# Performance work log

Hardware: AMD Instinct MI355X
Metric: run time of the kernel (lower is better)

## Reference

```python
import jax, jax.numpy as jnp
import numpy as np

B, L, H, N, CIN, COUT, U = 32, 12, 12, 2048, 2, 1, 64
K3 = 3  # num_matrices = n_supports * max_diffusion_step + 1 = 1*2 + 1


def setup_inputs() -> dict:
    rng = np.random.default_rng(0)
    # random sparse-ish symmetric adjacency -> scaled laplacian support (lambda_max ~= 2)
    A = rng.random((N, N), dtype=np.float32)
    A = np.maximum(A, A.T)
    A = A * (A > 0.995)
    d = A.sum(axis=1)
    dis = 1.0 / np.sqrt(np.maximum(d, 1e-6))
    Lap = np.eye(N, dtype=np.float32) - (dis[:, None] * A) * dis[None, :]
    support = (Lap - np.eye(N, dtype=np.float32)).astype(np.float32)  # 2/lmax*L - I with lmax=2

    key = jax.random.key(0)
    ks = jax.random.split(key, 6)

    def w(k, shape, fan):
        return jax.random.normal(k, shape, jnp.float32) / np.float32(np.sqrt(fan))

    Cg_e = (CIN + U) * K3   # 198
    Cg_d = (COUT + U) * K3  # 195
    return {
        "history_data": jax.random.normal(ks[0], (B, L, N, CIN), jnp.float32),
        "support": jnp.asarray(support),
        "enc_Wg": w(ks[1], (Cg_e, 2 * U), Cg_e),
        "enc_bg": jnp.ones((2 * U,), jnp.float32),  # gate bias starts at 1.0 (original repo)
        "enc_Wc": w(ks[2], (Cg_e, U), Cg_e),
        "enc_bc": jnp.zeros((U,), jnp.float32),
        "dec_Wg": w(ks[3], (Cg_d, 2 * U), Cg_d),
        "dec_bg": jnp.ones((2 * U,), jnp.float32),
        "dec_Wc": w(ks[4], (Cg_d, U), Cg_d),
        "dec_bc": jnp.zeros((U,), jnp.float32),
        "Wp": w(ks[5], (U, COUT), U),
        "bp": jnp.zeros((COUT,), jnp.float32),
    }


def _gconv(support, x, W, b):
    # x: [B, N, C]; Chebyshev diffusion T0=x, T1=Sx, T2=2S(Sx)-x, stacked feature-major
    x1 = jnp.einsum('mn,bnc->bmc', support, x)
    x2 = 2.0 * jnp.einsum('mn,bnc->bmc', support, x1) - x
    xs = jnp.stack([x, x1, x2], axis=-1)  # [B, N, C, 3]
    b_, n_, c_, k_ = xs.shape
    y = xs.reshape(b_ * n_, c_ * k_) @ W + b
    return y.reshape(b_, n_, -1)


def _cell(support, x, h, Wg, bg, Wc, bc):
    # DCGRU cell: x [B,N,in], h [B,N,U]
    cat = jnp.concatenate([x, h], axis=-1)
    ru = jax.nn.sigmoid(_gconv(support, cat, Wg, bg))
    r, u = jnp.split(ru, 2, axis=-1)
    c = jnp.tanh(_gconv(support, jnp.concatenate([x, r * h], axis=-1), Wc, bc))
    return u * h + (1.0 - u) * c


def reference(history_data, support, enc_Wg, enc_bg, enc_Wc, enc_bc,
              dec_Wg, dec_bg, dec_Wc, dec_bc, Wp, bp):
    hist = jnp.transpose(history_data, (1, 0, 2, 3))  # [L, B, N, CIN]
    h0 = jnp.zeros((B, N, U), history_data.dtype)

    def enc_step(h, xt):
        return _cell(support, xt, h, enc_Wg, enc_bg, enc_Wc, enc_bc), None

    h_enc, _ = jax.lax.scan(enc_step, h0, hist)

    go = jnp.zeros((B, N, COUT), history_data.dtype)

    def dec_step(carry, _):
        h, xin = carry
        h = _cell(support, xin, h, dec_Wg, dec_bg, dec_Wc, dec_bc)
        out = (h.reshape(-1, U) @ Wp + bp).reshape(B, N, COUT)
        return (h, out), out

    _, outs = jax.lax.scan(dec_step, (h_enc, go), None, length=H)  # [H, B, N, COUT]
    return jnp.transpose(outs, (1, 0, 2, 3))  # [B, H, N, COUT]
```

## Files before the change

### kernel.cpp

```cpp
#include <hip/hip_runtime.h>
#include <math.h>

#define NN 2048
#define BB 32
#define LL 12
#define HHH 12
#define UU 64
#define STR 68
#define SLAB (BB*STR)
#define SEGS 8
#define SEGW (SLAB/SEGS)
#define MR (NN*BB)
#define CSR_CAP 262144
#define PACK_HALF 28672

typedef short bfrag __attribute__((ext_vector_type(8)));
typedef float ffrag __attribute__((ext_vector_type(4)));

__device__ __forceinline__ float sigm(float x) { return 1.0f / (1.0f + __expf(-x)); }
__device__ __forceinline__ float tanhfast(float x) {
  float e = __expf(2.0f * x);
  return 1.0f - 2.0f / (e + 1.0f);
}

__device__ __forceinline__ void cvt8(const float* a, bfrag* hi, bfrag* lo) {
  bfrag H, L;
  #pragma unroll
  for (int j = 0; j < 8; ++j) {
    unsigned u = __float_as_uint(a[j]);
    unsigned hb = (u + 0x7FFFu + ((u >> 16) & 1u)) >> 16;
    float rem = a[j] - __uint_as_float(hb << 16);
    unsigned u2 = __float_as_uint(rem);
    unsigned lb = (u2 + 0x7FFFu + ((u2 >> 16) & 1u)) >> 16;
    H[j] = (short)hb; L[j] = (short)lb;
  }
  *hi = H; *lo = L;
}

__global__ __launch_bounds__(256) void k_row_count(const float* __restrict__ S, int* __restrict__ cnt) {
  int m = blockIdx.x;
  const float* row = S + (size_t)m * NN;
  int c = 0;
  for (int i = threadIdx.x; i < NN; i += 256) c += (row[i] != 0.0f);
  __shared__ int sm[4];
  for (int off = 32; off; off >>= 1) c += __shfl_down(c, off, 64);
  if ((threadIdx.x & 63) == 0) sm[threadIdx.x >> 6] = c;
  __syncthreads();
  if (threadIdx.x == 0) cnt[m] = sm[0] + sm[1] + sm[2] + sm[3];
}

__global__ __launch_bounds__(256) void k_scan(const int* __restrict__ cnt, int* __restrict__ rp) {
  __shared__ int tot[256];
  int t = threadIdx.x;
  int base = t * 8;
  int v[8]; int s = 0;
  #pragma unroll
  for (int k = 0; k < 8; ++k) { v[k] = cnt[base + k]; s += v[k]; }
  tot[t] = s;
  __syncthreads();
  for (int off = 1; off < 256; off <<= 1) {
    int add = (t >= off) ? tot[t - off] : 0;
    __syncthreads();
    tot[t] += add;
    __syncthreads();
  }
  int run = (t == 0) ? 0 : tot[t - 1];
  #pragma unroll
  for (int k = 0; k < 8; ++k) { rp[base + k] = run; run += v[k]; }
  if (t == 255) rp[NN] = run;
}

__global__ __launch_bounds__(256) void k_fill(const float* __restrict__ S, const int* __restrict__ rp,
                                              int* __restrict__ cols, float* __restrict__ vals) {
  int m = blockIdx.x;
  const float* row = S + (size_t)m * NN;
  __shared__ int wsum[4];
  __shared__ int chunkbase;
  if (threadIdx.x == 0) chunkbase = rp[m];
  __syncthreads();
  int lane = threadIdx.x & 63, w = threadIdx.x >> 6;
  for (int ch = 0; ch < NN / 256; ++ch) {
    int i = ch * 256 + threadIdx.x;
    float val = row[i];
    bool p = (val != 0.0f);
    unsigned long long mask = __ballot(p);
    int rank = __popcll(mask & ((1ull << lane) - 1ull));
    if (lane == 0) wsum[w] = __popcll(mask);
    __syncthreads();
    int off = 0;
    for (int q = 0; q < w; ++q) off += wsum[q];
    if (p) { int k = chunkbase + off + rank; cols[k] = i * SLAB; vals[k] = val; }
    __syncthreads();
    if (threadIdx.x == 0) chunkbase += wsum[0] + wsum[1] + wsum[2] + wsum[3];
    __syncthreads();
  }
}

__global__ __launch_bounds__(256) void k_pack(const float* __restrict__ Wsrc, unsigned short* __restrict__ dst,
                                              int CIN_, int NO) {
  int idx = blockIdx.x * 256 + threadIdx.x;
  int nh_count = NO >> 6;
  int tot = nh_count * 7 * 4 * 64 * 8;
  if (idx >= tot) return;
  int j = idx & 7;
  int r1 = idx >> 3;  int lane = r1 & 63;
  int r2 = r1 >> 6;   int nf = r2 & 3;
  int r3 = r2 >> 2;   int ks = r3 % 7; int nh = r3 / 7;
  int grp = lane >> 4, l15 = lane & 15;
  int col = nh*64 + nf*16 + l15;
  float wv = 0.0f;
  int kb = -1, c = 0;
  if (ks < 6) {
    kb = ks >> 1;
    c = CIN_ + (ks & 1)*32 + grp*8 + j;
  } else {
    int q = grp*8 + j;
    if (q < 3*CIN_) { kb = q / CIN_; c = q % CIN_; }
  }
  if (kb >= 0) {
    float w0 = Wsrc[((size_t)c*3 + 0)*NO + col];
    float w1 = Wsrc[((size_t)c*3 + 1)*NO + col];
    float w2 = Wsrc[((size_t)c*3 + 2)*NO + col];
    wv = (kb == 0) ? (w0 - w2) : ((kb == 1) ? w1 : 2.0f*w2);
  }
  unsigned u = __float_as_uint(wv);
  unsigned hb = (u + 0x7FFFu + ((u >> 16) & 1u)) >> 16;
  float rem = wv - __uint_as_float(hb << 16);
  unsigned u2 = __float_as_uint(rem);
  unsigned lb = (u2 + 0x7FFFu + ((u2 >> 16) & 1u)) >> 16;
  size_t basehi = ((size_t)nh*PACK_HALF) + ((((size_t)ks*4 + nf)*2 + 0)*64 + lane)*8 + j;
  size_t baselo = ((size_t)nh*PACK_HALF) + ((((size_t)ks*4 + nf)*2 + 1)*64 + lane)*8 + j;
  dst[basehi] = (unsigned short)hb;
  dst[baselo] = (unsigned short)lb;
}

__global__ __launch_bounds__(256) void k_setx(const float* __restrict__ hist, float* __restrict__ cat, int t) {
  int idx = blockIdx.x * 256 + threadIdx.x;
  if (idx >= MR * 2) return;
  int c = idx & 1, row = idx >> 1;
  int n = row >> 5, b = row & 31;
  cat[(size_t)row * STR + 64 + c] = hist[(((size_t)(b * LL + t)) * NN + n) * 2 + c];
}

__global__ __launch_bounds__(320) void k_hop(
    const int* __restrict__ rp, const int* __restrict__ colsS, const float* __restrict__ vals,
    const float* __restrict__ src, float* __restrict__ Y) {
  int orig = blockIdx.x;
  int seg = orig & 7;
  int pair = orig >> 3;
  int nodeA = pair * 2, nodeB = nodeA + 1;
  int tid = threadIdx.x;
  if (tid >= SEGW) return;
  int w0 = seg * SEGW + tid;
  int ja  = __builtin_amdgcn_readfirstlane(rp[nodeA]);
  int ja1 = __builtin_amdgcn_readfirstlane(rp[nodeA + 1]);
  int jb  = ja1;
  int jb1 = __builtin_amdgcn_readfirstlane(rp[nodeB + 1]);
  float accA0 = 0.f, accA1 = 0.f, accB0 = 0.f, accB1 = 0.f;

  while (ja + 4 <= ja1 && jb + 4 <= jb1) {
    int   oa0 = colsS[ja],   oa1 = colsS[ja+1], oa2 = colsS[ja+2], oa3 = colsS[ja+3];
    int   ob0 = colsS[jb],   ob1 = colsS[jb+1], ob2 = colsS[jb+2], ob3 = colsS[jb+3];
    float sa0 = vals[ja],    sa1 = vals[ja+1],  sa2 = vals[ja+2],  sa3 = vals[ja+3];
    float sb0 = vals[jb],    sb1 = vals[jb+1],  sb2 = vals[jb+2],  sb3 = vals[jb+3];
    float va0 = src[oa0 + w0], va1 = src[oa1 + w0], va2 = src[oa2 + w0], va3 = src[oa3 + w0];
    float vb0 = src[ob0 + w0], vb1 = src[ob1 + w0], vb2 = src[ob2 + w0], vb3 = src[ob3 + w0];
    accA0 = fmaf(sa0, va0, accA0); accA1 = fmaf(sa1, va1, accA1);
    accA0 = fmaf(sa2, va2, accA0); accA1 = fmaf(sa3, va3, accA1);
    accB0 = fmaf(sb0, vb0, accB0); accB1 = fmaf(sb1, vb1, accB1);
    accB0 = fmaf(sb2, vb2, accB0); accB1 = fmaf(sb3, vb3, accB1);
    ja += 4; jb += 4;
  }
  for (; ja + 4 <= ja1; ja += 4) {
    int   o0 = colsS[ja],  o1 = colsS[ja+1], o2 = colsS[ja+2], o3 = colsS[ja+3];
    float s0 = vals[ja],   s1 = vals[ja+1],  s2 = vals[ja+2],  s3 = vals[ja+3];
    float v0 = src[o0 + w0], v1 = src[o1 + w0], v2 = src[o2 + w0], v3 = src[o3 + w0];
    accA0 = fmaf(s0, v0, accA0); accA1 = fmaf(s1, v1, accA1);
    accA0 = fmaf(s2, v2, accA0); accA1 = fmaf(s3, v3, accA1);
  }
  for (; ja < ja1; ++ja) accA0 = fmaf(vals[ja], src[colsS[ja] + w0], accA0);
  for (; jb + 4 <= jb1; jb += 4) {
    int   o0 = colsS[jb],  o1 = colsS[jb+1], o2 = colsS[jb+2], o3 = colsS[jb+3];
    float s0 = vals[jb],   s1 = vals[jb+1],  s2 = vals[jb+2],  s3 = vals[jb+3];
    float v0 = src[o0 + w0], v1 = src[o1 + w0], v2 = src[o2 + w0], v3 = src[o3 + w0];
    accB0 = fmaf(s0, v0, accB0); accB1 = fmaf(s1, v1, accB1);
    accB0 = fmaf(s2, v2, accB0); accB1 = fmaf(s3, v3, accB1);
  }
  for (; jb < jb1; ++jb) accB0 = fmaf(vals[jb], src[colsS[jb] + w0], accB0);

  Y[(size_t)nodeA * SLAB + w0] = accA0 + accA1;
  Y[(size_t)nodeB * SLAB + w0] = accB0 + accB1;
}

__device__ __forceinline__ int rowOf(int chunk, int s, int lr) {
  return (chunk * 32 + (lr >> 2)) * BB + s * 4 + (lr & 3);
}

template<int CATM>
__global__ __launch_bounds__(512, 4) void k_gate(
    const float* __restrict__ catP, const float* __restrict__ T1P, const float* __restrict__ T2P,
    const unsigned short* __restrict__ Bpack, const float* __restrict__ bg,
    float* __restrict__ zP, float* __restrict__ Ug) {
  __shared__ __align__(16) unsigned short Bl[PACK_HALF];
  int tid = threadIdx.x;
  int bid = blockIdx.x;
  int s = bid & 7;
  int nfh = (bid >> 3) & 1;
  int chunk = bid >> 4;
  int w = tid >> 6, lane = tid & 63, grp = lane >> 4, l15 = lane & 15;
  int row0 = rowOf(chunk, s, w*16 + l15);

  float av[7][8];
  #pragma unroll
  for (int ks = 0; ks < 6; ++ks) {
    const float* p0 = (ks < 2) ? catP : ((ks < 4) ? T1P : T2P);
    const float* a0 = p0 + (size_t)row0*STR + (ks & 1)*32 + grp*8;
    *(float4*)(av[ks])     = *(const float4*)a0;
    *(float4*)(av[ks] + 4) = *(const float4*)(a0 + 4);
  }
  #pragma unroll
  for (int j2 = 0; j2 < 8; ++j2) av[6][j2] = 0.f;
  if (grp == 0) {
    size_t rb = (size_t)row0*STR + 64;
    if (CATM == 1) {
      av[6][0] = catP[rb];  av[6][1] = catP[rb + 1];
      av[6][2] = T1P[rb];   av[6][3] = T1P[rb + 1];
      av[6][4] = T2P[rb];   av[6][5] = T2P[rb + 1];
    } else {
      av[6][0] = catP[rb];
      av[6][1] = T1P[rb];
      av[6][2] = T2P[rb];
    }
  }

  {
    const float4* srcv = (const float4*)(Bpack + (size_t)nfh * PACK_HALF);
    float4* dstv = (float4*)Bl;
    #pragma unroll
    for (int i = 0; i < 7; ++i) dstv[tid + 512*i] = srcv[tid + 512*i];
  }
  __syncthreads();

  ffrag acc[4];
  #pragma unroll
  for (int nf = 0; nf < 4; ++nf) acc[nf] = (ffrag){0.f, 0.f, 0.f, 0.f};
  #pragma unroll
  for (int ks = 0; ks < 7; ++ks) {
    bfrag ah0, al0;
    cvt8(av[ks], &ah0, &al0);
    #pragma unroll
    for (int nf = 0; nf < 4; ++nf) {
      const unsigned short* bb = Bl + (((size_t)(ks*4 + nf)*2)*64 + lane)*8;
      bfrag bh = *(const bfrag*)bb;
      bfrag bl = *(const bfrag*)(bb + 512);
      acc[nf] = __builtin_amdgcn_mfma_f32_16x16x32_bf16(ah0, bh, acc[nf], 0, 0, 0);
      acc[nf] = __builtin_amdgcn_mfma_f32_16x16x32_bf16(ah0, bl, acc[nf], 0, 0, 0);
      acc[nf] = __builtin_amdgcn_mfma_f32_16x16x32_bf16(al0, bh, acc[nf], 0, 0, 0);
    }
  }
  float bgv[4];
  #pragma unroll
  for (int nf = 0; nf < 4; ++nf) bgv[nf] = bg[nfh*64 + nf*16 + l15];
  #pragma unroll
  for (int reg = 0; reg < 4; ++reg) {
    int row = rowOf(chunk, s, w*16 + grp*4 + reg);
    #pragma unroll
    for (int nf = 0; nf < 4; ++nf) {
      int col = nf*16 + l15;
      float v = sigm(acc[nf][reg] + bgv[nf]);
      if (nfh == 0) {
        float ho = catP[(size_t)row*STR + col];
        zP[(size_t)row*STR + col] = v * ho;
      } else {
        Ug[(size_t)row*UU + col] = v;
      }
    }
  }
  if (nfh == 0 && l15 == 0) {
    #pragma unroll
    for (int reg = 0; reg < 4; ++reg) {
      int row = rowOf(chunk, s, w*16 + grp*4 + reg);
      size_t zb = (size_t)row*STR;
      zP[zb + 64] = catP[zb + 64];
      zP[zb + 65] = (CATM == 1) ? catP[zb + 65] : 0.f;
      zP[zb + 66] = 0.f; zP[zb + 67] = 0.f;
    }
  }
}

template<bool DEC>
__global__ __launch_bounds__(512, 4) void k_cand(
    const float* __restrict__ zP, const float* __restrict__ T1P, const float* __restrict__ T2P,
    const unsigned short* __restrict__ Bpack, const float* __restrict__ bc,
    const float* __restrict__ Ug, const float* __restrict__ catCur,
    float* __restrict__ catNext,
    const float* __restrict__ Wp, const float* __restrict__ bp,
    float* __restrict__ out, const float* __restrict__ hist, int tpar) {
  __shared__ __align__(16) unsigned short Bl[PACK_HALF];
  int tid = threadIdx.x;
  int bid = blockIdx.x;
  int s = bid & 7;
  int chunk = bid >> 3;
  int w = tid >> 6, lane = tid & 63, grp = lane >> 4, l15 = lane & 15;
  int row0 = rowOf(chunk, s, w*16 + l15);

  float av[7][8];
  #pragma unroll
  for (int ks = 0; ks < 6; ++ks) {
    const float* p0 = (ks < 2) ? zP : ((ks < 4) ? T1P : T2P);
    const float* a0 = p0 + (size_t)row0*STR + (ks & 1)*32 + grp*8;
    *(float4*)(av[ks])     = *(const float4*)a0;
    *(float4*)(av[ks] + 4) = *(const float4*)(a0 + 4);
  }
  #pragma unroll
  for (int j2 = 0; j2 < 8; ++j2) av[6][j2] = 0.f;
  if (grp == 0) {
    size_t rb = (size_t)row0*STR + 64;
    if (!DEC) {
      av[6][0] = zP[rb];  av[6][1] = zP[rb + 1];
      av[6][2] = T1P[rb]; av[6][3] = T1P[rb + 1];
      av[6][4] = T2P[rb]; av[6][5] = T2P[rb + 1];
    } else {
      av[6][0] = zP[rb];
      av[6][1] = T1P[rb];
      av[6][2] = T2P[rb];
    }
  }

  {
    const float4* srcv = (const float4*)Bpack;
    float4* dstv = (float4*)Bl;
    #pragma unroll
    for (int i = 0; i < 7; ++i) dstv[tid + 512*i] = srcv[tid + 512*i];
  }
  __syncthreads();

  ffrag acc[4];
  #pragma unroll
  for (int nf = 0; nf < 4; ++nf) acc[nf] = (ffrag){0.f, 0.f, 0.f, 0.f};
  #pragma unroll
  for (int ks = 0; ks < 7; ++ks) {
    bfrag ah0, al0;
    cvt8(av[ks], &ah0, &al0);
    #pragma unroll
    for (int nf = 0; nf < 4; ++nf) {
      const unsigned short* bb = Bl + (((size_t)(ks*4 + nf)*2)*64 + lane)*8;
      bfrag bh = *(const bfrag*)bb;
      bfrag bl = *(const bfrag*)(bb + 512);
      acc[nf] = __builtin_amdgcn_mfma_f32_16x16x32_bf16(ah0, bh, acc[nf], 0, 0, 0);
      acc[nf] = __builtin_amdgcn_mfma_f32_16x16x32_bf16(ah0, bl, acc[nf], 0, 0, 0);
      acc[nf] = __builtin_amdgcn_mfma_f32_16x16x32_bf16(al0, bh, acc[nf], 0, 0, 0);
    }
  }
  float bcv[4], wpv[4];
  #pragma unroll
  for (int nf = 0; nf < 4; ++nf) {
    bcv[nf] = bc[nf*16 + l15];
    wpv[nf] = DEC ? Wp[nf*16 + l15] : 0.f;
  }
  float bp0 = DEC ? bp[0] : 0.f;
  #pragma unroll
  for (int reg = 0; reg < 4; ++reg) {
    int row = rowOf(chunk, s, w*16 + grp*4 + reg);
    float p = 0.f;
    #pragma unroll
    for (int nf = 0; nf < 4; ++nf) {
      int col = nf*16 + l15;
      float cf = tanhfast(acc[nf][reg] + bcv[nf]);
      float u  = Ug[(size_t)row*UU + col];
      float ho = catCur[(size_t)row*STR + col];
      float hv = u * ho + (1.0f - u) * cf;
      catNext[(size_t)row*STR + col] = hv;
      if (DEC) p = fmaf(hv, wpv[nf], p);
    }
    if (DEC) {
      p += __shfl_xor(p, 1, 64);
      p += __shfl_xor(p, 2, 64);
      p += __shfl_xor(p, 4, 64);
      p += __shfl_xor(p, 8, 64);
      if (l15 == 0) {
        float val = p + bp0;
        int n = row >> 5, b = row & 31;
        out[((size_t)b*HHH + tpar)*NN + n] = val;
        catNext[(size_t)row*STR + 64] = val;
        catNext[(size_t)row*STR + 65] = 0.f;
      }
    } else {
      if (l15 == 0) {
        int n = row >> 5, b = row & 31;
        bool hv2 = tpar < LL;
        const float* hx = hist + (((size_t)(b*LL + tpar)) * NN + n) * 2;
        catNext[(size_t)row*STR + 64] = hv2 ? hx[0] : 0.f;
        catNext[(size_t)row*STR + 65] = hv2 ? hx[1] : 0.f;
      }
    }
  }
}

extern "C" void kernel_launch(void* const* d_in, const int* in_sizes, int n_in,
                              void* d_out, int out_size, void* d_ws, size_t ws_size,
                              hipStream_t stream) {
  (void)in_sizes; (void)n_in; (void)out_size; (void)ws_size;
  const float* hist = (const float*)d_in[0];
  const float* support = (const float*)d_in[1];
  const float* eWg = (const float*)d_in[2];
  const float* ebg = (const float*)d_in[3];
  const float* eWc = (const float*)d_in[4];
  const float* ebc = (const float*)d_in[5];
  const float* dWg = (const float*)d_in[6];
  const float* dbg = (const float*)d_in[7];
  const float* dWc = (const float*)d_in[8];
  const float* dbc = (const float*)d_in[9];
  const float* Wp  = (const float*)d_in[10];
  const float* bp  = (const float*)d_in[11];
  float* out = (float*)d_out;

  char* base = (char*)d_ws;
  size_t off = 0;
  auto carve = [&](size_t bytes) -> void* {
    void* p = base + off;
    off += (bytes + 255) & ~(size_t)255;
    return p;
  };
  int*   cnt   = (int*)carve(NN * 4);
  int*   rpB   = (int*)carve((NN + 1) * 4);
  int*   colsB = (int*)carve(CSR_CAP * 4);
  float* valsB = (float*)carve(CSR_CAP * 4);
  unsigned short* Pge = (unsigned short*)carve(2 * PACK_HALF * 2);
  unsigned short* Pgd = (unsigned short*)carve(2 * PACK_HALF * 2);
  unsigned short* Pce = (unsigned short*)carve((size_t)PACK_HALF * 2);
  unsigned short* Pcd = (unsigned short*)carve((size_t)PACK_HALF * 2);
  float* T1P  = (float*)carve((size_t)NN * SLAB * 4);
  float* T2P  = (float*)carve((size_t)NN * SLAB * 4);
  float* zP   = (float*)carve((size_t)NN * SLAB * 4);
  float* UgF  = (float*)carve((size_t)MR * UU * 4);
  float* catA = (float*)carve((size_t)NN * SLAB * 4);
  float* catB = (float*)carve((size_t)NN * SLAB * 4);

  hipMemsetAsync(catA, 0, (size_t)NN * SLAB * 4, stream);
  hipMemsetAsync(catB, 0, (size_t)NN * SLAB * 4, stream);

  k_row_count<<<NN, 256, 0, stream>>>(support, cnt);
  k_scan<<<1, 256, 0, stream>>>(cnt, rpB);
  k_fill<<<NN, 256, 0, stream>>>(support, rpB, colsB, valsB);
  k_pack<<<112, 256, 0, stream>>>(eWg, Pge, 2, 128);
  k_pack<<<56, 256, 0, stream>>>(eWc, Pce, 2, 64);
  k_pack<<<112, 256, 0, stream>>>(dWg, Pgd, 1, 128);
  k_pack<<<56, 256, 0, stream>>>(dWc, Pcd, 1, 64);
  k_setx<<<(MR*2 + 255)/256, 256, 0, stream>>>(hist, catA, 0);

  float* hc = catA; float* hn = catB;
  for (int t = 0; t < LL; ++t) {
    k_hop<<<NN*SEGS/2, 320, 0, stream>>>(rpB, colsB, valsB, hc, T1P);
    k_hop<<<NN*SEGS/2, 320, 0, stream>>>(rpB, colsB, valsB, T1P, T2P);
    k_gate<1><<<1024, 512, 0, stream>>>(hc, T1P, T2P, Pge, ebg, zP, UgF);
    k_hop<<<NN*SEGS/2, 320, 0, stream>>>(rpB, colsB, valsB, zP, T1P);
    k_hop<<<NN*SEGS/2, 320, 0, stream>>>(rpB, colsB, valsB, T1P, T2P);
    k_cand<false><<<512, 512, 0, stream>>>(zP, T1P, T2P, Pce, ebc, UgF, hc, hn,
                                           Wp, bp, out, hist, t + 1);
    float* tmp = hc; hc = hn; hn = tmp;
  }
  for (int t = 0; t < HHH; ++t) {
    k_hop<<<NN*SEGS/2, 320, 0, stream>>>(rpB, colsB, valsB, hc, T1P);
    k_hop<<<NN*SEGS/2, 320, 0, stream>>>(rpB, colsB, valsB, T1P, T2P);
    k_gate<2><<<1024, 512, 0, stream>>>(hc, T1P, T2P, Pgd, dbg, zP, UgF);
    k_hop<<<NN*SEGS/2, 320, 0, stream>>>(rpB, colsB, valsB, zP, T1P);
    k_hop<<<NN*SEGS/2, 320, 0, stream>>>(rpB, colsB, valsB, T1P, T2P);
    k_cand<true><<<512, 512, 0, stream>>>(zP, T1P, T2P, Pcd, dbc, UgF, hc, hn,
                                          Wp, bp, out, hist, t);
    float* tmp = hc; hc = hn; hn = tmp;
  }
}
```

Measured before the change: 3.901 ms.

## Process multiple row chunks per gate/cand block with double-buffered A loads

```diff
diff --git a/kernel.cpp b/kernel.cpp
--- a/kernel.cpp
+++ b/kernel.cpp
@@ -197,20 +197,9 @@
 }
 
 template<int CATM>
-__global__ __launch_bounds__(512, 4) void k_gate(
-    const float* __restrict__ catP, const float* __restrict__ T1P, const float* __restrict__ T2P,
-    const unsigned short* __restrict__ Bpack, const float* __restrict__ bg,
-    float* __restrict__ zP, float* __restrict__ Ug) {
-  __shared__ __align__(16) unsigned short Bl[PACK_HALF];
-  int tid = threadIdx.x;
-  int bid = blockIdx.x;
-  int s = bid & 7;
-  int nfh = (bid >> 3) & 1;
-  int chunk = bid >> 4;
-  int w = tid >> 6, lane = tid & 63, grp = lane >> 4, l15 = lane & 15;
-  int row0 = rowOf(chunk, s, w*16 + l15);
-
-  float av[7][8];
+__device__ __forceinline__ void loadA_gate(const float* __restrict__ catP, const float* __restrict__ T1P,
+                                           const float* __restrict__ T2P, int row0, int grp,
+                                           float (&av)[7][8]) {
   #pragma unroll
   for (int ks = 0; ks < 6; ++ks) {
     const float* p0 = (ks < 2) ? catP : ((ks < 4) ? T1P : T2P);
@@ -232,16 +221,10 @@
       av[6][2] = T2P[rb];
     }
   }
-
-  {
-    const float4* srcv = (const float4*)(Bpack + (size_t)nfh * PACK_HALF);
-    float4* dstv = (float4*)Bl;
-    #pragma unroll
-    for (int i = 0; i < 7; ++i) dstv[tid + 512*i] = srcv[tid + 512*i];
-  }
-  __syncthreads();
-
-  ffrag acc[4];
+}
+
+__device__ __forceinline__ void gemm7(const float (&av)[7][8], const unsigned short* __restrict__ Bl,
+                                      int lane, ffrag (&acc)[4]) {
   #pragma unroll
   for (int nf = 0; nf < 4; ++nf) acc[nf] = (ffrag){0.f, 0.f, 0.f, 0.f};
   #pragma unroll
@@ -258,38 +241,76 @@
       acc[nf] = __builtin_amdgcn_mfma_f32_16x16x32_bf16(al0, bh, acc[nf], 0, 0, 0);
     }
   }
+}
+
+template<int CATM>
+__global__ __launch_bounds__(512, 2) void k_gate(
+    const float* __restrict__ catP, const float* __restrict__ T1P, const float* __restrict__ T2P,
+    const unsigned short* __restrict__ Bpack, const float* __restrict__ bg,
+    float* __restrict__ zP, float* __restrict__ Ug) {
+  __shared__ __align__(16) unsigned short Bl[PACK_HALF];
+  int tid = threadIdx.x;
+  int bid = blockIdx.x;
+  int s = bid & 7;
+  int nfh = (bid >> 3) & 1;
+  int gb = bid >> 4;
+  int w = tid >> 6, lane = tid & 63, grp = lane >> 4, l15 = lane & 15;
+  int lr = w*16 + l15;
+
+  float avA[7][8], avB[7][8];
+  loadA_gate<CATM>(catP, T1P, T2P, rowOf(gb, s, lr), grp, avA);
+  {
+    const float4* srcv = (const float4*)(Bpack + (size_t)nfh * PACK_HALF);
+    float4* dstv = (float4*)Bl;
+    #pragma unroll
+    for (int i = 0; i < 7; ++i) dstv[tid + 512*i] = srcv[tid + 512*i];
+  }
+  __syncthreads();
+
   float bgv[4];
   #pragma unroll
   for (int nf = 0; nf < 4; ++nf) bgv[nf] = bg[nfh*64 + nf*16 + l15];
-  #pragma unroll
-  for (int reg = 0; reg < 4; ++reg) {
-    int row = rowOf(chunk, s, w*16 + grp*4 + reg);
-    #pragma unroll
-    for (int nf = 0; nf < 4; ++nf) {
-      int col = nf*16 + l15;
-      float v = sigm(acc[nf][reg] + bgv[nf]);
-      if (nfh == 0) {
-        float ho = catP[(size_t)row*STR + col];
-        zP[(size_t)row*STR + col] = v * ho;
-      } else {
-        Ug[(size_t)row*UU + col] = v;
-      }
-    }
-  }
-  if (nfh == 0 && l15 == 0) {
+
+  auto epi = [&](const ffrag (&acc)[4], int chunk) {
     #pragma unroll
     for (int reg = 0; reg < 4; ++reg) {
       int row = rowOf(chunk, s, w*16 + grp*4 + reg);
-      size_t zb = (size_t)row*STR;
-      zP[zb + 64] = catP[zb + 64];
-      zP[zb + 65] = (CATM == 1) ? catP[zb + 65] : 0.f;
-      zP[zb + 66] = 0.f; zP[zb + 67] = 0.f;
+      #pragma unroll
+      for (int nf = 0; nf < 4; ++nf) {
+        int col = nf*16 + l15;
+        float v = sigm(acc[nf][reg] + bgv[nf]);
+        if (nfh == 0) {
+          float ho = catP[(size_t)row*STR + col];
+          zP[(size_t)row*STR + col] = v * ho;
+        } else {
+          Ug[(size_t)row*UU + col] = v;
+        }
+      }
     }
-  }
+    if (nfh == 0 && l15 == 0) {
+      #pragma unroll
+      for (int reg = 0; reg < 4; ++reg) {
+        int row = rowOf(chunk, s, w*16 + grp*4 + reg);
+        size_t zb = (size_t)row*STR;
+        zP[zb + 64] = catP[zb + 64];
+        zP[zb + 65] = (CATM == 1) ? catP[zb + 65] : 0.f;
+        zP[zb + 66] = 0.f; zP[zb + 67] = 0.f;
+      }
+    }
+  };
+
+  ffrag acc[4];
+  loadA_gate<CATM>(catP, T1P, T2P, rowOf(gb + 16, s, lr), grp, avB);
+  gemm7(avA, Bl, lane, acc); epi(acc, gb);
+  loadA_gate<CATM>(catP, T1P, T2P, rowOf(gb + 32, s, lr), grp, avA);
+  gemm7(avB, Bl, lane, acc); epi(acc, gb + 16);
+  loadA_gate<CATM>(catP, T1P, T2P, rowOf(gb + 48, s, lr), grp, avB);
+  gemm7(avA, Bl, lane, acc); epi(acc, gb + 32);
+  gemm7(avB, Bl, lane, acc); epi(acc, gb + 48);
 }
 
 template<bool DEC>
-__global__ __launch_bounds__(512, 4) void k_cand(
+__global__ __launch_bounds__(512, 2) void k_cand(
     const float* __restrict__ zP, const float* __restrict__ T1P, const float* __restrict__ T2P,
     const unsigned short* __restrict__ Bpack, const float* __restrict__ bc,
     const float* __restrict__ Ug, const float* __restrict__ catCur,
@@ -300,33 +321,19 @@
   int tid = threadIdx.x;
   int bid = blockIdx.x;
   int s = bid & 7;
-  int chunk = bid >> 3;
+  int gb = bid >> 3;
   int w = tid >> 6, lane = tid & 63, grp = lane >> 4, l15 = lane & 15;
-  int row0 = rowOf(chunk, s, w*16 + l15);
-
-  float av[7][8];
-  #pragma unroll
-  for (int ks = 0; ks < 6; ++ks) {
-    const float* p0 = (ks < 2) ? zP : ((ks < 4) ? T1P : T2P);
-    const float* a0 = p0 + (size_t)row0*STR + (ks & 1)*32 + grp*8;
-    *(float4*)(av[ks])     = *(const float4*)a0;
-    *(float4*)(av[ks] + 4) = *(const float4*)(a0 + 4);
-  }
-  #pragma unroll
-  for (int j2 = 0; j2 < 8; ++j2) av[6][j2] = 0.f;
-  if (grp == 0) {
+  int lr = w*16 + l15;
+  const int CM = DEC ? 2 : 1;
+
+  float avA[7][8], avB[7][8];
+  loadA_gate<1>(zP, T1P, T2P, rowOf(gb, s, lr), grp, avA);
+  if (DEC && grp == 0) {
+    int row0 = rowOf(gb, s, lr);
     size_t rb = (size_t)row0*STR + 64;
-    if (!DEC) {
-      av[6][0] = zP[rb];  av[6][1] = zP[rb + 1];
-      av[6][2] = T1P[rb]; av[6][3] = T1P[rb + 1];
-      av[6][4] = T2P[rb]; av[6][5] = T2P[rb + 1];
-    } else {
-      av[6][0] = zP[rb];
-      av[6][1] = T1P[rb];
-      av[6][2] = T2P[rb];
-    }
-  }
-
+    avA[6][0] = zP[rb]; avA[6][1] = T1P[rb]; avA[6][2] = T2P[rb];
+    avA[6][3] = 0.f; avA[6][4] = 0.f; avA[6][5] = 0.f;
+  }
   {
     const float4* srcv = (const float4*)Bpack;
     float4* dstv = (float4*)Bl;
@@ -335,23 +342,6 @@
   }
   __syncthreads();
 
-  ffrag acc[4];
-  #pragma unroll
-  for (int nf = 0; nf < 4; ++nf) acc[nf] = (ffrag){0.f, 0.f, 0.f, 0.f};
-  #pragma unroll
-  for (int ks = 0; ks < 7; ++ks) {
-    bfrag ah0, al0;
-    cvt8(av[ks], &ah0, &al0);
-    #pragma unroll
-    for (int nf = 0; nf < 4; ++nf) {
-      const unsigned short* bb = Bl + (((size_t)(ks*4 + nf)*2)*64 + lane)*8;
-      bfrag bh = *(const bfrag*)bb;
-      bfrag bl = *(const bfrag*)(bb + 512);
-      acc[nf] = __builtin_amdgcn_mfma_f32_16x16x32_bf16(ah0, bh, acc[nf], 0, 0, 0);
-      acc[nf] = __builtin_amdgcn_mfma_f32_16x16x32_bf16(ah0, bl, acc[nf], 0, 0, 0);
-      acc[nf] = __builtin_amdgcn_mfma_f32_16x16x32_bf16(al0, bh, acc[nf], 0, 0, 0);
-    }
-  }
   float bcv[4], wpv[4];
   #pragma unroll
   for (int nf = 0; nf < 4; ++nf) {
@@ -359,42 +349,57 @@
     wpv[nf] = DEC ? Wp[nf*16 + l15] : 0.f;
   }
   float bp0 = DEC ? bp[0] : 0.f;
-  #pragma unroll
-  for (int reg = 0; reg < 4; ++reg) {
-    int row = rowOf(chunk, s, w*16 + grp*4 + reg);
-    float p = 0.f;
+
+  auto epi = [&](const ffrag (&acc)[4], int chunk) {
     #pragma unroll
-    for (int nf = 0; nf < 4; ++nf) {
-      int col = nf*16 + l15;
-      float cf = tanhfast(acc[nf][reg] + bcv[nf]);
-      float u  = Ug[(size_t)row*UU + col];
-      float ho = catCur[(size_t)row*STR + col];
-      float hv = u * ho + (1.0f - u) * cf;
-      catNext[(size_t)row*STR + col] = hv;
-      if (DEC) p = fmaf(hv, wpv[nf], p);
-    }
-    if (DEC) {
-      p += __shfl_xor(p, 1, 64);
-      p += __shfl_xor(p, 2, 64);
-      p += __shfl_xor(p, 4, 64);
-      p += __shfl_xor(p, 8, 64);
-      if (l15 == 0) {
-        float val = p + bp0;
-        int n = row >> 5, b = row & 31;
-        out[((size_t)b*HHH + tpar)*NN + n] = val;
-        catNext[(size_t)row*STR + 64] = val;
-        catNext[(size_t)row*STR + 65] = 0.f;
+    for (int reg = 0; reg < 4; ++reg) {
+      int row = rowOf(chunk, s, w*16 + grp*4 + reg);
+      float p = 0.f;
+      #pragma unroll
+      for (int nf = 0; nf < 4; ++nf) {
+        int col = nf*16 + l15;
+        float cf = tanhfast(acc[nf][reg] + bcv[nf]);
+        float u  = Ug[(size_t)row*UU + col];
+        float ho = catCur[(size_t)row*STR + col];
+        float hv = u * ho + (1.0f - u) * cf;
+        catNext[(size_t)row*STR + col] = hv;
+        if (DEC) p = fmaf(hv, wpv[nf], p);
       }
-    } else {
-      if (l15 == 0) {
-        int n = row >> 5, b = row & 31;
-        bool hv2 = tpar < LL;
-        const float* hx = hist + (((size_t)(b*LL + tpar)) * NN + n) * 2;
-        catNext[(size_t)row*STR + 64] = hv2 ? hx[0] : 0.f;
-        catNext[(size_t)row*STR + 65] = hv2 ? hx[1] : 0.f;
+      if (DEC) {
+        p += __shfl_xor(p, 1, 64);
+        p += __shfl_xor(p, 2, 64);
+        p += __shfl_xor(p, 4, 64);
+        p += __shfl_xor(p, 8, 64);
+        if (l15 == 0) {
+          float val = p + bp0;
+          int n = row >> 5, b = row & 31;
+          out[((size_t)b*HHH + tpar)*NN + n] = val;
+          catNext[(size_t)row*STR + 64] = val;
+          catNext[(size_t)row*STR + 65] = 0.f;
+        }
+      } else {
+        if (l15 == 0) {
+          int n = row >> 5, b = row & 31;
+          bool hv2 = tpar < LL;
+          const float* hx = hist + (((size_t)(b*LL + tpar)) * NN + n) * 2;
+          catNext[(size_t)row*STR + 64] = hv2 ? hx[0] : 0.f;
+          catNext[(size_t)row*STR + 65] = hv2 ? hx[1] : 0.f;
+        }
       }
     }
-  }
+  };
+
+  ffrag acc[4];
+  loadA_gate<1>(zP, T1P, T2P, rowOf(gb + 32, s, lr), grp, avB);
+  if (DEC && grp == 0) {
+    int row1 = rowOf(gb + 32, s, lr);
+    size_t rb = (size_t)row1*STR + 64;
+    avB[6][0] = zP[rb]; avB[6][1] = T1P[rb]; avB[6][2] = T2P[rb];
+    avB[6][3] = 0.f; avB[6][4] = 0.f; avB[6][5] = 0.f;
+  }
+  gemm7(avA, Bl, lane, acc); epi(acc, gb);
+  gemm7(avB, Bl, lane, acc); epi(acc, gb + 32);
+  (void)CM;
 }
 
 extern "C" void kernel_launch(void* const* d_in, const int* in_sizes, int n_in,
@@ -453,20 +458,20 @@
   for (int t = 0; t < LL; ++t) {
     k_hop<<<NN*SEGS/2, 320, 0, stream>>>(rpB, colsB, valsB, hc, T1P);
     k_hop<<<NN*SEGS/2, 320, 0, stream>>>(rpB, colsB, valsB, T1P, T2P);
-    k_gate<1><<<1024, 512, 0, stream>>>(hc, T1P, T2P, Pge, ebg, zP, UgF);
+    k_gate<1><<<256, 512, 0, stream>>>(hc, T1P, T2P, Pge, ebg, zP, UgF);
     k_hop<<<NN*SEGS/2, 320, 0, stream>>>(rpB, colsB, valsB, zP, T1P);
     k_hop<<<NN*SEGS/2, 320, 0, stream>>>(rpB, colsB, valsB, T1P, T2P);
-    k_cand<false><<<512, 512, 0, stream>>>(zP, T1P, T2P, Pce, ebc, UgF, hc, hn,
+    k_cand<false><<<256, 512, 0, stream>>>(zP, T1P, T2P, Pce, ebc, UgF, hc, hn,
                                            Wp, bp, out, hist, t + 1);
     float* tmp = hc; hc = hn; hn = tmp;
   }
   for (int t = 0; t < HHH; ++t) {
     k_hop<<<NN*SEGS/2, 320, 0, stream>>>(rpB, colsB, valsB, hc, T1P);
     k_hop<<<NN*SEGS/2, 320, 0, stream>>>(rpB, colsB, valsB, T1P, T2P);
-    k_gate<2><<<1024, 512, 0, stream>>>(hc, T1P, T2P, Pgd, dbg, zP, UgF);
+    k_gate<2><<<256, 512, 0, stream>>>(hc, T1P, T2P, Pgd, dbg, zP, UgF);
     k_hop<<<NN*SEGS/2, 320, 0, stream>>>(rpB, colsB, valsB, zP, T1P);
     k_hop<<<NN*SEGS/2, 320, 0, stream>>>(rpB, colsB, valsB, T1P, T2P);
-    k_cand<true><<<512, 512, 0, stream>>>(zP, T1P, T2P, Pcd, dbc, UgF, hc, hn,
+    k_cand<true><<<256, 512, 0, stream>>>(zP, T1P, T2P, Pcd, dbc, UgF, hc, hn,
                                           Wp, bp, out, hist, t);
     float* tmp = hc; hc = hn; hn = tmp;
   }
```

Measured after the change: 4.262 ms. 1.09x slower.
